# Optimization experiments

Hardware: AMD Instinct MI355X
Metric: run time of the kernel (lower is better)

The kernel has to match this reference:

```python
import jax, jax.numpy as jnp
import numpy as np

D_MODEL = 1024
NUM_HEADS = 16
BATCH = 2
SEQ = 2048


def _trunc_normal(key, shape, std):
    # truncated normal on [-3std, 3std], matching torch.nn.init.trunc_normal_
    return jax.random.truncated_normal(key, -3.0, 3.0, shape, dtype=jnp.float32) * std


def setup_inputs() -> dict:
    key = jax.random.key(0)
    kx, kq, kk, kv, ko = jax.random.split(key, 5)
    std = (2.0 / (D_MODEL + D_MODEL)) ** 0.5
    return {
        "X": jax.random.normal(kx, (BATCH, SEQ, D_MODEL), dtype=jnp.float32),
        "q_proj": _trunc_normal(kq, (D_MODEL, D_MODEL), std),
        "k_proj": _trunc_normal(kk, (D_MODEL, D_MODEL), std),
        "v_proj": _trunc_normal(kv, (D_MODEL, D_MODEL), std),
        "o_proj": _trunc_normal(ko, (D_MODEL, D_MODEL), std),
    }


def reference(X, q_proj, k_proj, v_proj, o_proj):
    B, S, D = X.shape
    H = NUM_HEADS
    d_k = D // H

    # weights stored as (d_model, d_model); split output dim into heads
    q_w = q_proj.reshape(H, d_k, D)        # heads d_k d_model
    k_w = k_proj.reshape(H, d_k, D)
    v_w = v_proj.reshape(H, d_k, D)
    o_w = o_proj.reshape(D, H, d_k).transpose(1, 0, 2)  # heads d_model d_v

    q = jnp.einsum('hkd,bsd->bhsk', q_w, X)  # [B,H,S,d_k]
    k = jnp.einsum('hkd,bsd->bhsk', k_w, X)
    v = jnp.einsum('hkd,bsd->bhsk', v_w, X)

    scale = 1.0 / jnp.sqrt(jnp.asarray(d_k, dtype=X.dtype))
    scores = jnp.einsum('bhqk,bhsk->bhqs', q, k) * scale  # [B,H,S,S]
    causal = jnp.tril(jnp.ones((S, S), dtype=bool))
    scores = jnp.where(causal, scores, jnp.asarray(-jnp.inf, dtype=scores.dtype))
    attn = jax.nn.softmax(scores, axis=-1)
    attn_out = jnp.einsum('bhqs,bhsk->bhqk', attn, v)  # [B,H,S,d_v]

    return jnp.einsum('hdv,bhsv->bsd', o_w, attn_out)  # [B,S,d_model]
```

## Files before the change

### kernel.cpp

```cpp
#include <hip/hip_runtime.h>

typedef unsigned short u16;
typedef __bf16 bf16x8 __attribute__((ext_vector_type(8)));
typedef float f32x4 __attribute__((ext_vector_type(4)));
typedef u16 u16x8 __attribute__((ext_vector_type(8)));
typedef u16 u16x4v __attribute__((ext_vector_type(4)));

#define D_MODEL 1024
#define SEQ 2048
#define NB 2
#define NH 16

#define MFMA(a, b, c) __builtin_amdgcn_mfma_f32_16x16x32_bf16(a, b, c, 0, 0, 0)

__device__ __forceinline__ u16 f2bf(float f) {
  unsigned u = __builtin_bit_cast(unsigned, f);
  u += 0x7FFFu + ((u >> 16) & 1u);
  return (u16)(u >> 16);
}

__device__ __forceinline__ u16 f2bf_hw(float f) {
  return __builtin_bit_cast(u16, (__bf16)f);
}

__device__ __forceinline__ bf16x8 ld8(const u16* p) {
  return __builtin_bit_cast(bf16x8, *(const u16x8*)p);
}

typedef const __attribute__((address_space(1))) unsigned gu32;
typedef __attribute__((address_space(3))) unsigned lu32;
__device__ __forceinline__ void gload16(const u16* g, u16* l) {
  __builtin_amdgcn_global_load_lds((gu32*)g, (lu32*)l, 16, 0, 0);
}

__global__ __launch_bounds__(256) void convert_kernel(
    const float* __restrict__ X, const float* __restrict__ Wq,
    const float* __restrict__ Wk, const float* __restrict__ Wv,
    const float* __restrict__ Wo, u16* __restrict__ Xb, u16* __restrict__ Wb)
{
  const int NX4 = 1024 * 1024;
  const int NW4 = 256 * 1024;
  const int TOT = NX4 + 4 * NW4;
  for (int i = blockIdx.x * 256 + threadIdx.x; i < TOT; i += gridDim.x * 256) {
    const float* src;
    u16* dst;
    if (i < NX4) {
      src = X + (size_t)i * 4;
      dst = Xb + (size_t)i * 4;
    } else {
      int j = i - NX4;
      int w = j >> 18;
      int off = j & (NW4 - 1);
      const float* ws = (w == 0) ? Wq : (w == 1) ? Wk : (w == 2) ? Wv : Wo;
      src = ws + (size_t)off * 4;
      dst = Wb + (size_t)j * 4;
    }
    float4 v = *(const float4*)src;
    u16x4v o = { f2bf(v.x), f2bf(v.y), f2bf(v.z), f2bf(v.w) };
    *(u16x4v*)dst = o;
  }
}

template<int MODE>
__global__ __launch_bounds__(256) void gemm128(
    const u16* __restrict__ A, const u16* __restrict__ B,
    u16* __restrict__ Qb, u16* __restrict__ Kb, u16* __restrict__ Vt,
    float* __restrict__ out)
{
  __shared__ u16 As[128 * 64];
  __shared__ u16 Bs[128 * 64];
  const int t = threadIdx.x;
  const int lane = t & 63, w = t >> 6;
  const int wr = w >> 1, wc = w & 1;
  const int m0 = blockIdx.x * 128;
  const int n0 = blockIdx.y * 128;
  const int kg = lane >> 4, lr = lane & 15;
  const int lrow = lane >> 3, lch = lane & 7;

  f32x4 acc[4][4] = {};

  for (int kt = 0; kt < 16; ++kt) {
    __syncthreads();
    #pragma unroll
    for (int i = 0; i < 4; ++i) {
      int row = (w * 4 + i) * 8 + lrow;
      int sch = lch ^ (row & 7);
      gload16(&A[(size_t)(m0 + row) * 1024 + kt * 64 + sch * 8], &As[(w * 4 + i) * 512]);
      gload16(&B[(size_t)(n0 + row) * 1024 + kt * 64 + sch * 8], &Bs[(w * 4 + i) * 512]);
    }
    __syncthreads();

    #pragma unroll
    for (int kh = 0; kh < 2; ++kh) {
      bf16x8 a[4], b[4];
      #pragma unroll
      for (int mi = 0; mi < 4; ++mi) {
        int row = wr * 64 + mi * 16 + lr;
        int ch = (kh * 4 + kg) ^ (lr & 7);
        a[mi] = ld8(&As[row * 64 + ch * 8]);
      }
      #pragma unroll
      for (int ni = 0; ni < 4; ++ni) {
        int row = wc * 64 + ni * 16 + lr;
        int ch = (kh * 4 + kg) ^ (lr & 7);
        b[ni] = ld8(&Bs[row * 64 + ch * 8]);
      }
      #pragma unroll
      for (int mi = 0; mi < 4; ++mi)
        #pragma unroll
        for (int ni = 0; ni < 4; ++ni)
          acc[mi][ni] = MFMA(a[mi], b[ni], acc[mi][ni]);
    }
  }

  if (MODE == 0) {
    const int zby = blockIdx.y >> 3;
    const int nl0 = (blockIdx.y & 7) * 128;
    const float scl = (zby == 0) ? 0.125f : 1.0f;
    #pragma unroll
    for (int mi = 0; mi < 4; ++mi) {
      #pragma unroll
      for (int ni = 0; ni < 4; ++ni) {
        int m = m0 + wr * 64 + mi * 16 + kg * 4;
        int nl = nl0 + wc * 64 + ni * 16 + lr;
        int bb = m >> 11, s = m & (SEQ - 1);
        int h = nl >> 6, dk = nl & 63;
        size_t bh = (size_t)(bb * NH + h);
        if (zby == 2) {
          u16x4v v = { f2bf(acc[mi][ni][0]), f2bf(acc[mi][ni][1]),
                       f2bf(acc[mi][ni][2]), f2bf(acc[mi][ni][3]) };
          *(u16x4v*)&Vt[(bh * 64 + dk) * SEQ + s] = v;
        } else {
          u16* dst = (zby == 0 ? Qb : Kb) + ((bh * SEQ + s) * 64 + dk);
          #pragma unroll
          for (int i = 0; i < 4; ++i) dst[(size_t)i * 64] = f2bf(acc[mi][ni][i] * scl);
        }
      }
    }
  } else {
    #pragma unroll
    for (int mi = 0; mi < 4; ++mi) {
      #pragma unroll
      for (int ni = 0; ni < 4; ++ni) {
        int m = m0 + wr * 64 + mi * 16 + kg * 4;
        int n = n0 + wc * 64 + ni * 16 + lr;
        #pragma unroll
        for (int i = 0; i < 4; ++i)
          out[(size_t)(m + i) * D_MODEL + n] = acc[mi][ni][i];
      }
    }
  }
}

__global__ __launch_bounds__(256) void attn_kernel(
    const u16* __restrict__ Qb, const u16* __restrict__ Kb,
    const u16* __restrict__ Vt, u16* __restrict__ AO)
{
  __shared__ u16 Ks[2][64 * 64];
  __shared__ u16 Vs[2][64 * 64];
  __shared__ u16 Ps[4][16][72];
  const int t = threadIdx.x;
  const int bh = blockIdx.y;
  const int p = blockIdx.x;
  const int lane = t & 63, wv = t >> 6;
  const int kg = lane >> 4, lr = lane & 15;
  const int r8 = lane >> 3, c = lane & 7;
  const int b = bh >> 4, h = bh & (NH - 1);

  auto stage = [&](int buf, int kv0) {
    #pragma unroll
    for (int i = 0; i < 2; ++i) {
      int s = wv * 2 + i;
      int row = s * 8 + r8;
      int sc = c ^ (row & 7);
      gload16(&Kb[((size_t)bh * SEQ + kv0 + row) * 64 + sc * 8], &Ks[buf][s * 512]);
      gload16(&Vt[((size_t)bh * 64 + row) * SEQ + kv0 + sc * 8], &Vs[buf][s * 512]);
    }
  };

  #pragma unroll 1
  for (int seg = 0; seg < 2; ++seg) {
    const int qt = seg ? (31 - p) : p;
    const int ntile = qt + 1;
    const int q0 = qt * 64;

    const size_t qrow = (size_t)bh * SEQ + q0 + wv * 16 + lr;
    bf16x8 aq0 = ld8(&Qb[qrow * 64 + kg * 8]);
    bf16x8 aq1 = ld8(&Qb[qrow * 64 + 32 + kg * 8]);

    f32x4 of[4] = {};
    float rs[4] = {0.f, 0.f, 0.f, 0.f};

    __syncthreads();
    stage(0, 0);
    int cur = 0;

    for (int kt = 0; kt < ntile; ++kt) {
      const int kv0 = kt * 64;
      __syncthreads();
      if (kt + 1 < ntile) stage(cur ^ 1, (kt + 1) * 64);

      const u16* kb = &Ks[cur][0];
      f32x4 sc4[4] = {};
      #pragma unroll
      for (int ct = 0; ct < 4; ++ct) {
        int ch0 = kg ^ (lr & 7);
        int ch1 = (4 + kg) ^ (lr & 7);
        sc4[ct] = MFMA(aq0, ld8(&kb[(ct * 16 + lr) * 64 + ch0 * 8]), sc4[ct]);
        sc4[ct] = MFMA(aq1, ld8(&kb[(ct * 16 + lr) * 64 + ch1 * 8]), sc4[ct]);
      }

      const bool domask = (kt == ntile - 1);
      #pragma unroll
      for (int ct = 0; ct < 4; ++ct)
        #pragma unroll
        for (int i = 0; i < 4; ++i) {
          float e = __expf(sc4[ct][i]);
          if (domask && (kv0 + ct * 16 + lr > q0 + wv * 16 + kg * 4 + i)) e = 0.f;
          sc4[ct][i] = e;
          rs[i] += e;
        }

      #pragma unroll
      for (int ct = 0; ct < 4; ++ct)
        #pragma unroll
        for (int i = 0; i < 4; ++i)
          Ps[wv][kg * 4 + i][ct * 16 + lr] = f2bf_hw(sc4[ct][i]);

      bf16x8 pa0 = ld8(&Ps[wv][lr][kg * 8]);
      bf16x8 pa1 = ld8(&Ps[wv][lr][32 + kg * 8]);

      const u16* vb = &Vs[cur][0];
      #pragma unroll
      for (int vt = 0; vt < 4; ++vt) {
        int ch0 = kg ^ (lr & 7);
        int ch1 = (4 + kg) ^ (lr & 7);
        of[vt] = MFMA(pa0, ld8(&vb[(vt * 16 + lr) * 64 + ch0 * 8]), of[vt]);
        of[vt] = MFMA(pa1, ld8(&vb[(vt * 16 + lr) * 64 + ch1 * 8]), of[vt]);
      }
      cur ^= 1;
    }

    #pragma unroll
    for (int off = 1; off < 16; off <<= 1)
      #pragma unroll
      for (int i = 0; i < 4; ++i)
        rs[i] += __shfl_xor(rs[i], off, 64);

    #pragma unroll
    for (int i = 0; i < 4; ++i) {
      float inv = 1.0f / rs[i];
      int s = q0 + wv * 16 + kg * 4 + i;
      size_t base = ((size_t)(b * SEQ + s)) * D_MODEL + h * 64 + lr;
      #pragma unroll
      for (int vt = 0; vt < 4; ++vt)
        AO[base + vt * 16] = f2bf_hw(of[vt][i] * inv);
    }
  }
}

extern "C" void kernel_launch(void* const* d_in, const int* in_sizes, int n_in,
                              void* d_out, int out_size, void* d_ws, size_t ws_size,
                              hipStream_t stream) {
  const float* X  = (const float*)d_in[0];
  const float* Wq = (const float*)d_in[1];
  const float* Wk = (const float*)d_in[2];
  const float* Wv = (const float*)d_in[3];
  const float* Wo = (const float*)d_in[4];
  float* out = (float*)d_out;

  u16* Xb = (u16*)d_ws;
  u16* Wb = Xb + (size_t)4096 * 1024;
  u16* Qb = Wb + (size_t)4096 * 1024;
  u16* Kb = Qb + (size_t)4096 * 1024;
  u16* Vt = Kb + (size_t)4096 * 1024;
  u16* AO = Vt + (size_t)4096 * 1024;

  convert_kernel<<<2048, 256, 0, stream>>>(X, Wq, Wk, Wv, Wo, Xb, Wb);
  gemm128<0><<<dim3(32, 24), 256, 0, stream>>>(Xb, Wb, Qb, Kb, Vt, nullptr);
  attn_kernel<<<dim3(16, 32), 256, 0, stream>>>(Qb, Kb, Vt, AO);
  gemm128<1><<<dim3(32, 8), 256, 0, stream>>>(AO, Wb + (size_t)3 * 1024 * 1024,
                                              nullptr, nullptr, nullptr, out);
}
```

Baseline: 120.9 us.

## Load K/V tiles directly from global into registers, drop LDS staging

The attention kernel no longer stages K and V tiles through double-buffered shared memory with block-wide barriers. Each wave now loads its MFMA operands straight from global memory into registers and prefetches the next K tile during the current iteration. The grid is also transposed so that blocks sharing a batch-head launch adjacently, which should improve L2 reuse of K/V. The cost is that each of the four waves loads the same K/V data separately from global/L2, multiplying memory traffic, and register pressure rises.

```diff
diff --git a/kernel.cpp b/kernel.cpp
--- a/kernel.cpp
+++ b/kernel.cpp
@@ -156,27 +156,16 @@
     const u16* __restrict__ Qb, const u16* __restrict__ Kb,
     const u16* __restrict__ Vt, u16* __restrict__ AO)
 {
-  __shared__ u16 Ks[2][64 * 64];
-  __shared__ u16 Vs[2][64 * 64];
   __shared__ u16 Ps[4][16][72];
   const int t = threadIdx.x;
-  const int bh = blockIdx.y;
-  const int p = blockIdx.x;
+  const int bh = blockIdx.x;
+  const int p = blockIdx.y;
   const int lane = t & 63, wv = t >> 6;
   const int kg = lane >> 4, lr = lane & 15;
-  const int r8 = lane >> 3, c = lane & 7;
   const int b = bh >> 4, h = bh & (NH - 1);
 
-  auto stage = [&](int buf, int kv0) {
-    #pragma unroll
-    for (int i = 0; i < 2; ++i) {
-      int s = wv * 2 + i;
-      int row = s * 8 + r8;
-      int sc = c ^ (row & 7);
-      gload16(&Kb[((size_t)bh * SEQ + kv0 + row) * 64 + sc * 8], &Ks[buf][s * 512]);
-      gload16(&Vt[((size_t)bh * 64 + row) * SEQ + kv0 + sc * 8], &Vs[buf][s * 512]);
-    }
-  };
+  const u16* Kbase = Kb + (size_t)bh * SEQ * 64;
+  const u16* Vbase = Vt + (size_t)bh * 64 * SEQ;
 
   #pragma unroll 1
   for (int seg = 0; seg < 2; ++seg) {
@@ -191,23 +180,40 @@
     f32x4 of[4] = {};
     float rs[4] = {0.f, 0.f, 0.f, 0.f};
 
-    __syncthreads();
-    stage(0, 0);
-    int cur = 0;
-
+    bf16x8 kc0[4], kc1[4];
+    #pragma unroll
+    for (int ct = 0; ct < 4; ++ct) {
+      const u16* kp = Kbase + (size_t)(ct * 16 + lr) * 64 + kg * 8;
+      kc0[ct] = ld8(kp);
+      kc1[ct] = ld8(kp + 32);
+    }
+
+    #pragma unroll 1
     for (int kt = 0; kt < ntile; ++kt) {
       const int kv0 = kt * 64;
-      __syncthreads();
-      if (kt + 1 < ntile) stage(cur ^ 1, (kt + 1) * 64);
-
-      const u16* kb = &Ks[cur][0];
+
       f32x4 sc4[4] = {};
       #pragma unroll
       for (int ct = 0; ct < 4; ++ct) {
-        int ch0 = kg ^ (lr & 7);
-        int ch1 = (4 + kg) ^ (lr & 7);
-        sc4[ct] = MFMA(aq0, ld8(&kb[(ct * 16 + lr) * 64 + ch0 * 8]), sc4[ct]);
-        sc4[ct] = MFMA(aq1, ld8(&kb[(ct * 16 + lr) * 64 + ch1 * 8]), sc4[ct]);
+        sc4[ct] = MFMA(aq0, kc0[ct], sc4[ct]);
+        sc4[ct] = MFMA(aq1, kc1[ct], sc4[ct]);
+      }
+
+      bf16x8 vc0[4], vc1[4];
+      #pragma unroll
+      for (int vt = 0; vt < 4; ++vt) {
+        const u16* vp = Vbase + (size_t)(vt * 16 + lr) * SEQ + kv0 + kg * 8;
+        vc0[vt] = ld8(vp);
+        vc1[vt] = ld8(vp + 32);
+      }
+      bf16x8 kn0[4], kn1[4];
+      if (kt + 1 < ntile) {
+        #pragma unroll
+        for (int ct = 0; ct < 4; ++ct) {
+          const u16* kp = Kbase + (size_t)(kv0 + 64 + ct * 16 + lr) * 64 + kg * 8;
+          kn0[ct] = ld8(kp);
+          kn1[ct] = ld8(kp + 32);
+        }
       }
 
       const bool domask = (kt == ntile - 1);
@@ -230,15 +236,14 @@
       bf16x8 pa0 = ld8(&Ps[wv][lr][kg * 8]);
       bf16x8 pa1 = ld8(&Ps[wv][lr][32 + kg * 8]);
 
-      const u16* vb = &Vs[cur][0];
       #pragma unroll
       for (int vt = 0; vt < 4; ++vt) {
-        int ch0 = kg ^ (lr & 7);
-        int ch1 = (4 + kg) ^ (lr & 7);
-        of[vt] = MFMA(pa0, ld8(&vb[(vt * 16 + lr) * 64 + ch0 * 8]), of[vt]);
-        of[vt] = MFMA(pa1, ld8(&vb[(vt * 16 + lr) * 64 + ch1 * 8]), of[vt]);
-      }
-      cur ^= 1;
+        of[vt] = MFMA(pa0, vc0[vt], of[vt]);
+        of[vt] = MFMA(pa1, vc1[vt], of[vt]);
+      }
+
+      #pragma unroll
+      for (int ct = 0; ct < 4; ++ct) { kc0[ct] = kn0[ct]; kc1[ct] = kn1[ct]; }
     }
 
     #pragma unroll
@@ -278,7 +283,7 @@
 
   convert_kernel<<<2048, 256, 0, stream>>>(X, Wq, Wk, Wv, Wo, Xb, Wb);
   gemm128<0><<<dim3(32, 24), 256, 0, stream>>>(Xb, Wb, Qb, Kb, Vt, nullptr);
-  attn_kernel<<<dim3(16, 32), 256, 0, stream>>>(Qb, Kb, Vt, AO);
+  attn_kernel<<<dim3(32, 16), 256, 0, stream>>>(Qb, Kb, Vt, AO);
   gemm128<1><<<dim3(32, 8), 256, 0, stream>>>(AO, Wb + (size_t)3 * 1024 * 1024,
                                               nullptr, nullptr, nullptr, out);
 }
```

After: 195.1 us. 1.61x slower.
